# Optimization experiments

Hardware: AMD Instinct MI355X
Metric: run time of the kernel (lower is better)

The kernel has to match this reference:

```python
import jax, jax.numpy as jnp
from jax import lax
import numpy as np

DIM = 256
RES = 32          # D = H = W
HEADS = 8
HD = DIM // HEADS
SPLIT = 8
H_SP, W_SP = RES, SPLIT   # idx = 0: full-height stripe windows
SCALE = HD ** -0.5
B = 2
L = RES ** 3


def setup_inputs() -> dict:
    key = jax.random.key(0)
    k1, k2, k3 = jax.random.split(key, 3)
    qkv = jax.random.normal(k1, (3, B, L, DIM), dtype=jnp.float32)
    conv_w = jax.random.normal(k2, (DIM, 1, 3, 3), dtype=jnp.float32) * 0.1  # depthwise OIHW, groups=DIM
    conv_b = jax.random.normal(k3, (DIM,), dtype=jnp.float32) * 0.01
    return {"qkv": qkv, "conv_w": conv_w, "conv_b": conv_b}


def _to_window_imgs(x):
    # x: (B, L, C) -> per-depth-slice window images (Nw, C, H_sp, W_sp)
    Bc, Lc, C = x.shape
    nH, nW = RES // H_SP, RES // W_SP
    x = x.transpose(0, 2, 1).reshape(Bc, C, RES, nH, H_SP, nW, W_SP)      # B C D nH Hsp nW Wsp
    x = x.transpose(0, 2, 3, 5, 1, 4, 6)                                   # B D nH nW C Hsp Wsp
    return x.reshape(-1, C, H_SP, W_SP)


def _img_to_heads(xw):
    # (Nw, C, Hsp, Wsp) -> (Nw, heads, S, hd)
    return xw.reshape(-1, HEADS, HD, H_SP * W_SP).transpose(0, 1, 3, 2)


def reference(qkv, conv_w, conv_b):
    q, k, v = qkv[0], qkv[1], qkv[2]
    Bc, Lc, C = q.shape
    nH, nW = RES // H_SP, RES // W_SP

    qw = _img_to_heads(_to_window_imgs(q)) * SCALE    # (Nw, h, S, hd)
    kw = _img_to_heads(_to_window_imgs(k))
    vimg = _to_window_imgs(v)                          # (Nw, C, Hsp, Wsp)

    # LePE: depthwise 3x3 conv on v window images
    lepe = lax.conv_general_dilated(
        vimg, conv_w, window_strides=(1, 1), padding='SAME',
        feature_group_count=C,
        dimension_numbers=('NCHW', 'OIHW', 'NCHW')) + conv_b[None, :, None, None]
    lepe = _img_to_heads(lepe)                         # (Nw, h, S, hd)
    vw = _img_to_heads(vimg)

    attn = jax.nn.softmax(jnp.einsum('whsd,whtd->whst', qw, kw), axis=-1)
    x = jnp.einsum('whst,whtd->whsd', attn, vw) + lepe  # (Nw, h, S, hd)

    # windows -> image -> (B, L, C)
    x = x.transpose(0, 2, 1, 3).reshape(-1, H_SP * W_SP, C)               # (Nw, S, C)
    x = x.reshape(Bc, RES, nH, nW, H_SP, W_SP, C)
    x = x.transpose(0, 1, 2, 4, 3, 5, 6).reshape(Bc, RES, RES, RES, C)
    return x.reshape(Bc, -1, C)
```

## Files before the change

### kernel.cpp

```cpp
#include <hip/hip_runtime.h>
#include <hip/hip_bf16.h>
#include <stdint.h>


typedef short bf16x8 __attribute__((ext_vector_type(8)));
typedef float f32x4 __attribute__((ext_vector_type(4)));
typedef uint32_t u32x2 __attribute__((ext_vector_type(2)));
typedef uint32_t u32x4 __attribute__((ext_vector_type(4)));

#define KSTR 40
#define VSTR 264

__device__ __forceinline__ float bf2f_lo(uint32_t u) {
    union { uint32_t i; float f; } x; x.i = u << 16; return x.f;
}
__device__ __forceinline__ float bf2f_hi(uint32_t u) {
    union { uint32_t i; float f; } x; x.i = u & 0xffff0000u; return x.f;
}
__device__ __forceinline__ uint32_t cvt2(float a, float b) {
    union { __hip_bfloat162 h; uint32_t u; } x;
    x.h = __float22bfloat162_rn(make_float2(a, b));
    return x.u;
}

__global__ __launch_bounds__(256, 4)
void lepe_attn(const float* __restrict__ qkv,
               const float* __restrict__ conv_w,
               const float* __restrict__ conv_b,
               float* __restrict__ out)
{
    __shared__ uint16_t k_lds[256 * KSTR];
    __shared__ uint16_t vt_lds[32 * VSTR];
    __shared__ float w_lds[288];
    __shared__ float b_lds[32];

    const int tid  = threadIdx.x;
    const int lane = tid & 63;
    const int wave = tid >> 6;
    const int l15  = lane & 15;
    const int quad = lane >> 4;

    const int blk  = blockIdx.x;
    const int head = blk & 7;
    const int wid  = blk >> 3;
    const int b    = wid >> 7;
    const int rem  = wid & 127;
    const int dpt  = rem >> 2;
    const int nw   = rem & 3;

    const long base_l = (long)dpt * 1024 + nw * 8;
    const int  hc     = head * 32;

    const float c1 = 0.17677669529663687f * 1.4426950408889634f;

    {
        const int  s = tid;
        const long l = base_l + (s >> 3) * 32 + (s & 7);
        const float* kp = qkv + (((long)(2 + b) * 32768 + l) * 256 + hc);
        const float* vp = qkv + (((long)(4 + b) * 32768 + l) * 256 + hc);
        #pragma unroll
        for (int j = 0; j < 8; ++j) {
            float4 kv = ((const float4*)kp)[j];
            u32x2 kb = { cvt2(kv.x, kv.y), cvt2(kv.z, kv.w) };
            *(u32x2*)&k_lds[s * KSTR + j * 4] = kb;
            float4 vv = ((const float4*)vp)[j];
            uint32_t v01 = cvt2(vv.x, vv.y);
            uint32_t v23 = cvt2(vv.z, vv.w);
            vt_lds[(j * 4 + 0) * VSTR + s] = (uint16_t)v01;
            vt_lds[(j * 4 + 1) * VSTR + s] = (uint16_t)(v01 >> 16);
            vt_lds[(j * 4 + 2) * VSTR + s] = (uint16_t)v23;
            vt_lds[(j * 4 + 3) * VSTR + s] = (uint16_t)(v23 >> 16);
        }
        for (int i = tid; i < 288; i += 256) w_lds[i] = conv_w[head * 288 + i];
        if (tid < 32) b_lds[tid] = conv_b[hc + tid];
    }
    __syncthreads();

    const f32x4 zero4 = {0.f, 0.f, 0.f, 0.f};

    #pragma unroll 1
    for (int it = 0; it < 4; ++it) {
        const int rt = wave * 4 + it;

        const int  sq = rt * 16 + l15;
        const long ql = base_l + (sq >> 3) * 32 + (sq & 7);
        const float* qp = qkv + (((long)b * 32768 + ql) * 256 + hc + quad * 8);
        float4 q0 = ((const float4*)qp)[0];
        float4 q1 = ((const float4*)qp)[1];
        u32x4 qp4 = { cvt2(q0.x * c1, q0.y * c1), cvt2(q0.z * c1, q0.w * c1),
                      cvt2(q1.x * c1, q1.y * c1), cvt2(q1.z * c1, q1.w * c1) };
        const bf16x8 qfrag = __builtin_bit_cast(bf16x8, qp4);

        f32x4 accO[2] = {zero4, zero4};
        float ss0 = 0.f, ss1 = 0.f, ss2 = 0.f, ss3 = 0.f;

        #pragma unroll 1
        for (int qt = 0; qt < 4; ++qt) {
            f32x4 accS[4];
            __builtin_amdgcn_s_setprio(1);
            #pragma unroll
            for (int t = 0; t < 4; ++t) {
                const int tg = qt * 4 + t;
                bf16x8 afrag = *(const bf16x8*)&k_lds[(tg * 16 + l15) * KSTR + quad * 8];
                accS[t] = __builtin_amdgcn_mfma_f32_16x16x32_bf16(afrag, qfrag, zero4, 0, 0, 0);
            }
            __builtin_amdgcn_s_setprio(0);

            uint32_t pkl[4], pkh[4];
            #pragma unroll
            for (int t = 0; t < 4; ++t) {
                float p0 = exp2f(accS[t][0]);
                float p1 = exp2f(accS[t][1]);
                float p2 = exp2f(accS[t][2]);
                float p3 = exp2f(accS[t][3]);
                ss0 += p0; ss1 += p1; ss2 += p2; ss3 += p3;
                pkl[t] = cvt2(p0, p1);
                pkh[t] = cvt2(p2, p3);
            }

            __builtin_amdgcn_s_setprio(1);
            #pragma unroll
            for (int c = 0; c < 2; ++c) {
                uint32_t a0 = pkl[2 * c], a1 = pkl[2 * c + 1];
                uint32_t b0 = pkh[2 * c], b1 = pkh[2 * c + 1];
                asm("v_permlane32_swap_b32 %0, %1" : "+v"(a0), "+v"(a1));
                asm("v_permlane32_swap_b32 %0, %1" : "+v"(b0), "+v"(b1));
                asm("v_permlane16_swap_b32 %0, %1" : "+v"(a0), "+v"(a1));
                asm("v_permlane16_swap_b32 %0, %1" : "+v"(b0), "+v"(b1));
                u32x4 pv = {a0, b0, a1, b1};
                bf16x8 pa = __builtin_bit_cast(bf16x8, pv);
                const int kb = (qt * 2 + c) * 32 + quad * 8;
                bf16x8 vb0 = *(const bf16x8*)&vt_lds[l15 * VSTR + kb];
                accO[0] = __builtin_amdgcn_mfma_f32_16x16x32_bf16(pa, vb0, accO[0], 0, 0, 0);
                bf16x8 vb1 = *(const bf16x8*)&vt_lds[(16 + l15) * VSTR + kb];
                accO[1] = __builtin_amdgcn_mfma_f32_16x16x32_bf16(pa, vb1, accO[1], 0, 0, 0);
            }
            __builtin_amdgcn_s_setprio(0);
        }

        float ssum = (ss0 + ss1) + (ss2 + ss3);
        ssum += __shfl_xor(ssum, 16);
        ssum += __shfl_xor(ssum, 32);
        const float linv = __builtin_amdgcn_rcpf(ssum);
        float linv4[4];
        #pragma unroll
        for (int r = 0; r < 4; ++r) linv4[r] = __shfl(linv, quad * 4 + r);

        const int hrow = rt * 2 + (quad >> 1);
        const int wsel = quad & 1;
        #pragma unroll
        for (int n = 0; n < 2; ++n) {
            const int d = n * 16 + l15;
            const float* wrow = &w_lds[(n * 16 + l15) * 9];
            float lep0, lep1, lep2, lep3;
            lep0 = lep1 = lep2 = lep3 = b_lds[n * 16 + l15];
            #pragma unroll
            for (int dy = 0; dy < 3; ++dy) {
                const int hh = hrow + dy - 1;
                float e0 = 0.f, e1 = 0.f, e2 = 0.f, e3 = 0.f, e4 = 0.f, e5 = 0.f;
                if (hh >= 0 && hh < 32) {
                    uint4 rv = *(const uint4*)&vt_lds[d * VSTR + hh * 8];
                    float c0 = bf2f_lo(rv.x), c1v = bf2f_hi(rv.x);
                    float c2 = bf2f_lo(rv.y), c3 = bf2f_hi(rv.y);
                    float c4 = bf2f_lo(rv.z), c5 = bf2f_hi(rv.z);
                    float c6 = bf2f_lo(rv.w), c7 = bf2f_hi(rv.w);
                    e0 = wsel ? c3 : 0.f;  e1 = wsel ? c4 : c0;
                    e2 = wsel ? c5 : c1v;  e3 = wsel ? c6 : c2;
                    e4 = wsel ? c7 : c3;   e5 = wsel ? 0.f : c4;
                }
                const float w0 = wrow[dy * 3 + 0];
                const float w1 = wrow[dy * 3 + 1];
                const float w2 = wrow[dy * 3 + 2];
                lep0 = fmaf(w0, e0, fmaf(w1, e1, fmaf(w2, e2, lep0)));
                lep1 = fmaf(w0, e1, fmaf(w1, e2, fmaf(w2, e3, lep1)));
                lep2 = fmaf(w0, e2, fmaf(w1, e3, fmaf(w2, e4, lep2)));
                lep3 = fmaf(w0, e3, fmaf(w1, e4, fmaf(w2, e5, lep3)));
            }
            const float lp[4] = {lep0, lep1, lep2, lep3};
            #pragma unroll
            for (int r = 0; r < 4; ++r) {
                const int s  = rt * 16 + quad * 4 + r;
                const int h  = s >> 3, w_ = s & 7;
                const long ol = base_l + h * 32 + w_;
                out[((long)b * 32768 + ol) * 256 + hc + d] = accO[n][r] * linv4[r] + lp[r];
            }
        }
    }
}

extern "C" void kernel_launch(void* const* d_in, const int* in_sizes, int n_in,
                              void* d_out, int out_size, void* d_ws, size_t ws_size,
                              hipStream_t stream)
{
    const float* qkv = (const float*)d_in[0];
    const float* cw  = (const float*)d_in[1];
    const float* cb  = (const float*)d_in[2];
    float* o = (float*)d_out;
    lepe_attn<<<2048, 256, 0, stream>>>(qkv, cw, cb, o);
}
```

Baseline: 335.7 us.

## Remap block order, prefetch next Q tile, use raw exp2 intrinsic

Changes the block-index mapping so that consecutive blocks cover different windows for the same head group rather than all eight heads of one window, which alters memory access locality across concurrently running blocks. Prefetches the next iteration's Q rows into registers while the current tile is processed, hiding global load latency. Replaces exp2f with the raw hardware exp2 builtin, dropping the denormal/range handling. These cost a few extra registers and one redundant load on the last iteration.

```diff
diff --git a/kernel.cpp b/kernel.cpp
--- a/kernel.cpp
+++ b/kernel.cpp
@@ -41,8 +41,8 @@
     const int quad = lane >> 4;
 
     const int blk  = blockIdx.x;
-    const int head = blk & 7;
-    const int wid  = blk >> 3;
+    const int head = (blk >> 3) & 7;
+    const int wid  = ((blk >> 6) << 3) | (blk & 7);
     const int b    = wid >> 7;
     const int rem  = wid & 127;
     const int dpt  = rem >> 2;
@@ -78,18 +78,30 @@
 
     const f32x4 zero4 = {0.f, 0.f, 0.f, 0.f};
 
+    float4 qA0, qA1;
+    {
+        const int  sq = (wave * 4 + 0) * 16 + l15;
+        const long ql = base_l + (sq >> 3) * 32 + (sq & 7);
+        const float* qp = qkv + (((long)b * 32768 + ql) * 256 + hc + quad * 8);
+        qA0 = ((const float4*)qp)[0];
+        qA1 = ((const float4*)qp)[1];
+    }
+
     #pragma unroll 1
     for (int it = 0; it < 4; ++it) {
         const int rt = wave * 4 + it;
 
-        const int  sq = rt * 16 + l15;
-        const long ql = base_l + (sq >> 3) * 32 + (sq & 7);
-        const float* qp = qkv + (((long)b * 32768 + ql) * 256 + hc + quad * 8);
-        float4 q0 = ((const float4*)qp)[0];
-        float4 q1 = ((const float4*)qp)[1];
-        u32x4 qp4 = { cvt2(q0.x * c1, q0.y * c1), cvt2(q0.z * c1, q0.w * c1),
-                      cvt2(q1.x * c1, q1.y * c1), cvt2(q1.z * c1, q1.w * c1) };
+        u32x4 qp4 = { cvt2(qA0.x * c1, qA0.y * c1), cvt2(qA0.z * c1, qA0.w * c1),
+                      cvt2(qA1.x * c1, qA1.y * c1), cvt2(qA1.z * c1, qA1.w * c1) };
         const bf16x8 qfrag = __builtin_bit_cast(bf16x8, qp4);
+        {
+            const int  itn = (it < 3) ? it + 1 : 3;
+            const int  sq  = (wave * 4 + itn) * 16 + l15;
+            const long ql  = base_l + (sq >> 3) * 32 + (sq & 7);
+            const float* qp = qkv + (((long)b * 32768 + ql) * 256 + hc + quad * 8);
+            qA0 = ((const float4*)qp)[0];
+            qA1 = ((const float4*)qp)[1];
+        }
 
         f32x4 accO[2] = {zero4, zero4};
         float ss0 = 0.f, ss1 = 0.f, ss2 = 0.f, ss3 = 0.f;
@@ -109,10 +121,10 @@
             uint32_t pkl[4], pkh[4];
             #pragma unroll
             for (int t = 0; t < 4; ++t) {
-                float p0 = exp2f(accS[t][0]);
-                float p1 = exp2f(accS[t][1]);
-                float p2 = exp2f(accS[t][2]);
-                float p3 = exp2f(accS[t][3]);
+                float p0 = __builtin_amdgcn_exp2f(accS[t][0]);
+                float p1 = __builtin_amdgcn_exp2f(accS[t][1]);
+                float p2 = __builtin_amdgcn_exp2f(accS[t][2]);
+                float p3 = __builtin_amdgcn_exp2f(accS[t][3]);
                 ss0 += p0; ss1 += p1; ss2 += p2; ss3 += p3;
                 pkl[t] = cvt2(p0, p1);
                 pkh[t] = cvt2(p2, p3);
```

Result: faster. 321.6 us (-4.2%).

## Process two query tiles per wave, remap block-to-head order, use fast exp2

Applied to the files above, without the earlier changes.

Each wave now handles two 16-row query tiles at once, so every K and V fragment read from LDS feeds two MFMAs and there is more independent MFMA work to interleave. The KV loop is restructured into 8 steps of 32 keys, and the softmax uses the raw hardware exp2 builtin instead of exp2f. Block indices are remapped so that consecutive blocks cover 8 different windows of one head rather than 8 heads of one window, which changes the global memory access locality. The cost is higher register pressure under launch bounds of 4 blocks per CU, which may cause spills.

```diff
diff --git a/kernel.cpp b/kernel.cpp
--- a/kernel.cpp
+++ b/kernel.cpp
@@ -41,8 +41,8 @@
     const int quad = lane >> 4;
 
     const int blk  = blockIdx.x;
-    const int head = blk & 7;
-    const int wid  = blk >> 3;
+    const int head = (blk >> 3) & 7;
+    const int wid  = ((blk >> 6) << 3) | (blk & 7);
     const int b    = wid >> 7;
     const int rem  = wid & 127;
     const int dpt  = rem >> 2;
@@ -78,114 +78,158 @@
 
     const f32x4 zero4 = {0.f, 0.f, 0.f, 0.f};
 
+    #define EPILOG(RT, ACCO, LINV4) do {                                                   \
+        const int hrow = (RT) * 2 + (quad >> 1);                                           \
+        const int wsel = quad & 1;                                                         \
+        _Pragma("unroll")                                                                  \
+        for (int n = 0; n < 2; ++n) {                                                      \
+            const int d = n * 16 + l15;                                                    \
+            const float* wrow = &w_lds[(n * 16 + l15) * 9];                                \
+            float lep0, lep1, lep2, lep3;                                                  \
+            lep0 = lep1 = lep2 = lep3 = b_lds[n * 16 + l15];                               \
+            _Pragma("unroll")                                                              \
+            for (int dy = 0; dy < 3; ++dy) {                                               \
+                const int hh = hrow + dy - 1;                                              \
+                float e0 = 0.f, e1 = 0.f, e2 = 0.f, e3 = 0.f, e4 = 0.f, e5 = 0.f;          \
+                if (hh >= 0 && hh < 32) {                                                  \
+                    uint4 rv = *(const uint4*)&vt_lds[d * VSTR + hh * 8];                  \
+                    float c0 = bf2f_lo(rv.x), c1v = bf2f_hi(rv.x);                         \
+                    float c2 = bf2f_lo(rv.y), c3 = bf2f_hi(rv.y);                          \
+                    float c4 = bf2f_lo(rv.z), c5 = bf2f_hi(rv.z);                          \
+                    float c6 = bf2f_lo(rv.w), c7 = bf2f_hi(rv.w);                          \
+                    e0 = wsel ? c3 : 0.f;  e1 = wsel ? c4 : c0;                            \
+                    e2 = wsel ? c5 : c1v;  e3 = wsel ? c6 : c2;                            \
+                    e4 = wsel ? c7 : c3;   e5 = wsel ? 0.f : c4;                           \
+                }                                                                          \
+                const float w0 = wrow[dy * 3 + 0];                                         \
+                const float w1 = wrow[dy * 3 + 1];                                         \
+                const float w2 = wrow[dy * 3 + 2];                                         \
+                lep0 = fmaf(w0, e0, fmaf(w1, e1, fmaf(w2, e2, lep0)));                     \
+                lep1 = fmaf(w0, e1, fmaf(w1, e2, fmaf(w2, e3, lep1)));                     \
+                lep2 = fmaf(w0, e2, fmaf(w1, e3, fmaf(w2, e4, lep2)));                     \
+                lep3 = fmaf(w0, e3, fmaf(w1, e4, fmaf(w2, e5, lep3)));                     \
+            }                                                                              \
+            const float lp[4] = {lep0, lep1, lep2, lep3};                                  \
+            _Pragma("unroll")                                                              \
+            for (int r = 0; r < 4; ++r) {                                                  \
+                const int s  = (RT) * 16 + quad * 4 + r;                                   \
+                const int h  = s >> 3, w_ = s & 7;                                         \
+                const long ol = base_l + h * 32 + w_;                                      \
+                out[((long)b * 32768 + ol) * 256 + hc + d] = (ACCO)[n][r] * (LINV4)[r] + lp[r]; \
+            }                                                                              \
+        }                                                                                  \
+    } while (0)
+
     #pragma unroll 1
-    for (int it = 0; it < 4; ++it) {
-        const int rt = wave * 4 + it;
-
-        const int  sq = rt * 16 + l15;
-        const long ql = base_l + (sq >> 3) * 32 + (sq & 7);
-        const float* qp = qkv + (((long)b * 32768 + ql) * 256 + hc + quad * 8);
-        float4 q0 = ((const float4*)qp)[0];
-        float4 q1 = ((const float4*)qp)[1];
-        u32x4 qp4 = { cvt2(q0.x * c1, q0.y * c1), cvt2(q0.z * c1, q0.w * c1),
-                      cvt2(q1.x * c1, q1.y * c1), cvt2(q1.z * c1, q1.w * c1) };
-        const bf16x8 qfrag = __builtin_bit_cast(bf16x8, qp4);
-
-        f32x4 accO[2] = {zero4, zero4};
-        float ss0 = 0.f, ss1 = 0.f, ss2 = 0.f, ss3 = 0.f;
+    for (int itp = 0; itp < 2; ++itp) {
+        const int rtA = wave * 4 + itp * 2;
+        const int rtB = rtA + 1;
+
+        bf16x8 qfragA, qfragB;
+        {
+            const int  sqA = rtA * 16 + l15;
+            const long qlA = base_l + (sqA >> 3) * 32 + (sqA & 7);
+            const float* qpA = qkv + (((long)b * 32768 + qlA) * 256 + hc + quad * 8);
+            float4 a0 = ((const float4*)qpA)[0];
+            float4 a1 = ((const float4*)qpA)[1];
+            const int  sqB = rtB * 16 + l15;
+            const long qlB = base_l + (sqB >> 3) * 32 + (sqB & 7);
+            const float* qpB = qkv + (((long)b * 32768 + qlB) * 256 + hc + quad * 8);
+            float4 b0 = ((const float4*)qpB)[0];
+            float4 b1 = ((const float4*)qpB)[1];
+            u32x4 qa = { cvt2(a0.x * c1, a0.y * c1), cvt2(a0.z * c1, a0.w * c1),
+                         cvt2(a1.x * c1, a1.y * c1), cvt2(a1.z * c1, a1.w * c1) };
+            u32x4 qb = { cvt2(b0.x * c1, b0.y * c1), cvt2(b0.z * c1, b0.w * c1),
+                         cvt2(b1.x * c1, b1.y * c1), cvt2(b1.z * c1, b1.w * c1) };
+            qfragA = __builtin_bit_cast(bf16x8, qa);
+            qfragB = __builtin_bit_cast(bf16x8, qb);
+        }
+
+        f32x4 accOA[2] = {zero4, zero4};
+        f32x4 accOB[2] = {zero4, zero4};
+        float ssA0 = 0.f, ssA1 = 0.f, ssA2 = 0.f, ssA3 = 0.f;
+        float ssB0 = 0.f, ssB1 = 0.f, ssB2 = 0.f, ssB3 = 0.f;
 
         #pragma unroll 1
-        for (int qt = 0; qt < 4; ++qt) {
-            f32x4 accS[4];
+        for (int e = 0; e < 8; ++e) {
+            const int t0 = e * 2, t1 = e * 2 + 1;
+            bf16x8 afrag0 = *(const bf16x8*)&k_lds[(t0 * 16 + l15) * KSTR + quad * 8];
+            bf16x8 afrag1 = *(const bf16x8*)&k_lds[(t1 * 16 + l15) * KSTR + quad * 8];
             __builtin_amdgcn_s_setprio(1);
-            #pragma unroll
-            for (int t = 0; t < 4; ++t) {
-                const int tg = qt * 4 + t;
-                bf16x8 afrag = *(const bf16x8*)&k_lds[(tg * 16 + l15) * KSTR + quad * 8];
-                accS[t] = __builtin_amdgcn_mfma_f32_16x16x32_bf16(afrag, qfrag, zero4, 0, 0, 0);
-            }
+            f32x4 sA0 = __builtin_amdgcn_mfma_f32_16x16x32_bf16(afrag0, qfragA, zero4, 0, 0, 0);
+            f32x4 sB0 = __builtin_amdgcn_mfma_f32_16x16x32_bf16(afrag0, qfragB, zero4, 0, 0, 0);
+            f32x4 sA1 = __builtin_amdgcn_mfma_f32_16x16x32_bf16(afrag1, qfragA, zero4, 0, 0, 0);
+            f32x4 sB1 = __builtin_amdgcn_mfma_f32_16x16x32_bf16(afrag1, qfragB, zero4, 0, 0, 0);
             __builtin_amdgcn_s_setprio(0);
 
-            uint32_t pkl[4], pkh[4];
-            #pragma unroll
-            for (int t = 0; t < 4; ++t) {
-                float p0 = exp2f(accS[t][0]);
-                float p1 = exp2f(accS[t][1]);
-                float p2 = exp2f(accS[t][2]);
-                float p3 = exp2f(accS[t][3]);
-                ss0 += p0; ss1 += p1; ss2 += p2; ss3 += p3;
-                pkl[t] = cvt2(p0, p1);
-                pkh[t] = cvt2(p2, p3);
-            }
-
+            float pA00 = __builtin_amdgcn_exp2f(sA0[0]);
+            float pA01 = __builtin_amdgcn_exp2f(sA0[1]);
+            float pA02 = __builtin_amdgcn_exp2f(sA0[2]);
+            float pA03 = __builtin_amdgcn_exp2f(sA0[3]);
+            ssA0 += pA00; ssA1 += pA01; ssA2 += pA02; ssA3 += pA03;
+            float pA10 = __builtin_amdgcn_exp2f(sA1[0]);
+            float pA11 = __builtin_amdgcn_exp2f(sA1[1]);
+            float pA12 = __builtin_amdgcn_exp2f(sA1[2]);
+            float pA13 = __builtin_amdgcn_exp2f(sA1[3]);
+            ssA0 += pA10; ssA1 += pA11; ssA2 += pA12; ssA3 += pA13;
+            float pB00 = __builtin_amdgcn_exp2f(sB0[0]);
+            float pB01 = __builtin_amdgcn_exp2f(sB0[1]);
+            float pB02 = __builtin_amdgcn_exp2f(sB0[2]);
+            float pB03 = __builtin_amdgcn_exp2f(sB0[3]);
+            ssB0 += pB00; ssB1 += pB01; ssB2 += pB02; ssB3 += pB03;
+            float pB10 = __builtin_amdgcn_exp2f(sB1[0]);
+            float pB11 = __builtin_amdgcn_exp2f(sB1[1]);
+            float pB12 = __builtin_amdgcn_exp2f(sB1[2]);
+            float pB13 = __builtin_amdgcn_exp2f(sB1[3]);
+            ssB0 += pB10; ssB1 += pB11; ssB2 += pB12; ssB3 += pB13;
+
+            uint32_t a0 = cvt2(pA00, pA01), a1 = cvt2(pA10, pA11);
+            uint32_t a2 = cvt2(pA02, pA03), a3 = cvt2(pA12, pA13);
+            uint32_t b0 = cvt2(pB00, pB01), b1 = cvt2(pB10, pB11);
+            uint32_t b2 = cvt2(pB02, pB03), b3 = cvt2(pB12, pB13);
+            asm("v_permlane32_swap_b32 %0, %1" : "+v"(a0), "+v"(a1));
+            asm("v_permlane32_swap_b32 %0, %1" : "+v"(a2), "+v"(a3));
+            asm("v_permlane16_swap_b32 %0, %1" : "+v"(a0), "+v"(a1));
+            asm("v_permlane16_swap_b32 %0, %1" : "+v"(a2), "+v"(a3));
+            asm("v_permlane32_swap_b32 %0, %1" : "+v"(b0), "+v"(b1));
+            asm("v_permlane32_swap_b32 %0, %1" : "+v"(b2), "+v"(b3));
+            asm("v_permlane16_swap_b32 %0, %1" : "+v"(b0), "+v"(b1));
+            asm("v_permlane16_swap_b32 %0, %1" : "+v"(b2), "+v"(b3));
+            u32x4 pvA = {a0, a2, a1, a3};
+            u32x4 pvB = {b0, b2, b1, b3};
+            bf16x8 paA = __builtin_bit_cast(bf16x8, pvA);
+            bf16x8 paB = __builtin_bit_cast(bf16x8, pvB);
+
+            const int kb = e * 32 + quad * 8;
+            bf16x8 vb0 = *(const bf16x8*)&vt_lds[l15 * VSTR + kb];
+            bf16x8 vb1 = *(const bf16x8*)&vt_lds[(16 + l15) * VSTR + kb];
             __builtin_amdgcn_s_setprio(1);
-            #pragma unroll
-            for (int c = 0; c < 2; ++c) {
-                uint32_t a0 = pkl[2 * c], a1 = pkl[2 * c + 1];
-                uint32_t b0 = pkh[2 * c], b1 = pkh[2 * c + 1];
-                asm("v_permlane32_swap_b32 %0, %1" : "+v"(a0), "+v"(a1));
-                asm("v_permlane32_swap_b32 %0, %1" : "+v"(b0), "+v"(b1));
-                asm("v_permlane16_swap_b32 %0, %1" : "+v"(a0), "+v"(a1));
-                asm("v_permlane16_swap_b32 %0, %1" : "+v"(b0), "+v"(b1));
-                u32x4 pv = {a0, b0, a1, b1};
-                bf16x8 pa = __builtin_bit_cast(bf16x8, pv);
-                const int kb = (qt * 2 + c) * 32 + quad * 8;
-                bf16x8 vb0 = *(const bf16x8*)&vt_lds[l15 * VSTR + kb];
-                accO[0] = __builtin_amdgcn_mfma_f32_16x16x32_bf16(pa, vb0, accO[0], 0, 0, 0);
-                bf16x8 vb1 = *(const bf16x8*)&vt_lds[(16 + l15) * VSTR + kb];
-                accO[1] = __builtin_amdgcn_mfma_f32_16x16x32_bf16(pa, vb1, accO[1], 0, 0, 0);
-            }
+            accOA[0] = __builtin_amdgcn_mfma_f32_16x16x32_bf16(paA, vb0, accOA[0], 0, 0, 0);
+            accOB[0] = __builtin_amdgcn_mfma_f32_16x16x32_bf16(paB, vb0, accOB[0], 0, 0, 0);
+            accOA[1] = __builtin_amdgcn_mfma_f32_16x16x32_bf16(paA, vb1, accOA[1], 0, 0, 0);
+            accOB[1] = __builtin_amdgcn_mfma_f32_16x16x32_bf16(paB, vb1, accOB[1], 0, 0, 0);
             __builtin_amdgcn_s_setprio(0);
         }
 
-        float ssum = (ss0 + ss1) + (ss2 + ss3);
-        ssum += __shfl_xor(ssum, 16);
-        ssum += __shfl_xor(ssum, 32);
-        const float linv = __builtin_amdgcn_rcpf(ssum);
-        float linv4[4];
+        float ssumA = (ssA0 + ssA1) + (ssA2 + ssA3);
+        ssumA += __shfl_xor(ssumA, 16);
+        ssumA += __shfl_xor(ssumA, 32);
+        const float linvA = __builtin_amdgcn_rcpf(ssumA);
+        float ssumB = (ssB0 + ssB1) + (ssB2 + ssB3);
+        ssumB += __shfl_xor(ssumB, 16);
+        ssumB += __shfl_xor(ssumB, 32);
+        const float linvB = __builtin_amdgcn_rcpf(ssumB);
+        float linvA4[4], linvB4[4];
         #pragma unroll
-        for (int r = 0; r < 4; ++r) linv4[r] = __shfl(linv, quad * 4 + r);
-
-        const int hrow = rt * 2 + (quad >> 1);
-        const int wsel = quad & 1;
-        #pragma unroll
-        for (int n = 0; n < 2; ++n) {
-            const int d = n * 16 + l15;
-            const float* wrow = &w_lds[(n * 16 + l15) * 9];
-            float lep0, lep1, lep2, lep3;
-            lep0 = lep1 = lep2 = lep3 = b_lds[n * 16 + l15];
-            #pragma unroll
-            for (int dy = 0; dy < 3; ++dy) {
-                const int hh = hrow + dy - 1;
-                float e0 = 0.f, e1 = 0.f, e2 = 0.f, e3 = 0.f, e4 = 0.f, e5 = 0.f;
-                if (hh >= 0 && hh < 32) {
-                    uint4 rv = *(const uint4*)&vt_lds[d * VSTR + hh * 8];
-                    float c0 = bf2f_lo(rv.x), c1v = bf2f_hi(rv.x);
-                    float c2 = bf2f_lo(rv.y), c3 = bf2f_hi(rv.y);
-                    float c4 = bf2f_lo(rv.z), c5 = bf2f_hi(rv.z);
-                    float c6 = bf2f_lo(rv.w), c7 = bf2f_hi(rv.w);
-                    e0 = wsel ? c3 : 0.f;  e1 = wsel ? c4 : c0;
-                    e2 = wsel ? c5 : c1v;  e3 = wsel ? c6 : c2;
-                    e4 = wsel ? c7 : c3;   e5 = wsel ? 0.f : c4;
-                }
-                const float w0 = wrow[dy * 3 + 0];
-                const float w1 = wrow[dy * 3 + 1];
-                const float w2 = wrow[dy * 3 + 2];
-                lep0 = fmaf(w0, e0, fmaf(w1, e1, fmaf(w2, e2, lep0)));
-                lep1 = fmaf(w0, e1, fmaf(w1, e2, fmaf(w2, e3, lep1)));
-                lep2 = fmaf(w0, e2, fmaf(w1, e3, fmaf(w2, e4, lep2)));
-                lep3 = fmaf(w0, e3, fmaf(w1, e4, fmaf(w2, e5, lep3)));
-            }
-            const float lp[4] = {lep0, lep1, lep2, lep3};
-            #pragma unroll
-            for (int r = 0; r < 4; ++r) {
-                const int s  = rt * 16 + quad * 4 + r;
-                const int h  = s >> 3, w_ = s & 7;
-                const long ol = base_l + h * 32 + w_;
-                out[((long)b * 32768 + ol) * 256 + hc + d] = accO[n][r] * linv4[r] + lp[r];
-            }
-        }
+        for (int r = 0; r < 4; ++r) {
+            linvA4[r] = __shfl(linvA, quad * 4 + r);
+            linvB4[r] = __shfl(linvB, quad * 4 + r);
+        }
+
+        EPILOG(rtA, accOA, linvA4);
+        EPILOG(rtB, accOB, linvB4);
     }
+    #undef EPILOG
 }
 
 extern "C" void kernel_launch(void* const* d_in, const int* in_sizes, int n_in,
```

Result: faster. 319.3 us (-4.9%).
